# Optimization experiments

Hardware: AMD Instinct MI355X
Metric: run time of the kernel (lower is better)

Reference implementation:

```python
import jax, jax.numpy as jnp
import numpy as np

# hyperparameters (init_kwargs)
T = 0.1
MARGIN = 0.0
NEG_IOU = 0.5
K = 2              # pos_topk
WEIGHT = 1.0
EXPONENT = 2.0
NEG_SAMPLES = 512  # neg_samples_num
START_DNS_EPOCH = 1

# static problem sizes
B, SPB, TPS = 16, 2, 4          # videos, sentences/video, targets/sentence
N, C = 64, 256                  # clips, channels
S = B * SPB                     # total sentences = 32
M = S * TPS                     # total moments = 128


def setup_inputs() -> dict:
    key = jax.random.key(0)
    k1, k2, k3, k4 = jax.random.split(key, 4)
    return {
        "video_feats": jax.random.normal(k1, (S, C, N, N), jnp.float32),
        "sents_feats": jax.random.normal(k2, (S, C), jnp.float32),
        "num_sentences": jnp.full((B,), SPB, jnp.int32),
        "num_targets": jnp.full((S,), TPS, jnp.int32),
        "iou2d": jax.random.uniform(k3, (S, N, N), jnp.float32),
        "iou2ds": jax.random.uniform(k4, (M, N, N), jnp.float32),
        "mask2d": jnp.triu(jnp.ones((N, N), bool)),  # 2D-TAN valid-proposal mask
        "epoch": 2,
    }


def _normalize(x):
    return x / jnp.maximum(jnp.linalg.norm(x, axis=-1, keepdims=True), 1e-12)


def _loss_core(video_feats, sents_feats, iou2d, iou2ds,
               num_sentences, num_targets, mask2d, epoch):
    S_, C_, N_, _ = video_feats.shape
    B_ = num_sentences.shape[0]
    M_ = iou2ds.shape[0]
    P = N_ * (N_ + 1) // 2  # number of True in upper-triangular mask2d

    # masked_select(mask2d) -> gather flat proposal positions (static size P)
    flat_idx = jnp.nonzero(mask2d.reshape(-1), size=P)[0]
    vf = video_feats.reshape(S_, C_, N_ * N_)[:, :, flat_idx]        # (S,C,P)
    vf = _normalize(vf.transpose(0, 2, 1))                            # (S,P,C)
    _ = _normalize(sents_feats)                                       # normalized but unused downstream
    iou2d_f = iou2d.reshape(S_, -1)[:, flat_idx]                      # (S,P)
    iou2ds_f = iou2ds.reshape(M_, -1)[:, flat_idx]                    # (M,P)

    scatter_m2s = jnp.repeat(jnp.arange(S_), num_targets, total_repeat_length=M_)
    scatter_s2b = jnp.repeat(jnp.arange(B_), num_sentences, total_repeat_length=S_)
    scatter_b2s = jnp.concatenate([jnp.zeros((1,), jnp.int32),
                                   jnp.cumsum(num_sentences)[:-1].astype(jnp.int32)])

    # all (ref, pos) pairs within each sentence's num_targets*K topk slots (uniform -> static)
    nK = (M_ // S_) * K
    base = (jnp.arange(S_) * nK)[:, None, None]
    i = jnp.arange(nK)
    zero = jnp.zeros((nK,), jnp.int32)
    ref_idx = (base + i[None, :, None] + zero[None, None, :]).reshape(-1)   # (E,)
    pos_idx = (base + zero[None, :, None] + i[None, None, :]).reshape(-1)   # (E,)
    scatter_e2s = jnp.repeat(jnp.arange(S_), nK * nK)                        # (E,)

    # top-K proposals per moment by IoU
    topk_idx = jax.lax.top_k(iou2ds_f, K)[1]                                 # (M,K)
    allm = vf[scatter_m2s]                                                   # (M,P,C)
    topk_vf = jnp.take_along_axis(allm, topk_idx[:, :, None], axis=1)        # (M,K,C)
    pos_vf = topk_vf.reshape(M_ * K, C_)

    intra_pos = jnp.sum(pos_vf[ref_idx] * pos_vf[pos_idx], axis=-1)          # (E,)
    bank = vf[scatter_b2s].reshape(B_ * P, C_)                               # one sentence per video
    intra_all = pos_vf @ bank.T                                              # (M*K, B*P)

    # positive mask: own-video block, refined by iou2d > neg_iou
    own = scatter_s2b[:, None] == jnp.arange(B_)[None, :]                    # (S,B)
    s2v_pos = iou2d_f > NEG_IOU                                              # (S,P)
    pos_mask = jnp.where(own[:, :, None], s2v_pos[:, None, :], False).reshape(S_, B_ * P)

    if epoch >= START_DNS_EPOCH:
        # DNS: similarity-weighted negative sampling without replacement (Gumbel top-k)
        sim = (jnp.einsum('mkc,pc->mkp', topk_vf, bank).mean(axis=1) + 1.0) * 0.5   # (M,B*P)
        fused = jax.ops.segment_sum(sim, scatter_m2s, num_segments=S_)
        fused = fused / num_targets[:, None].astype(sim.dtype)                      # per-sentence mean
        fused = jnp.where(pos_mask, 0.0, fused ** EXPONENT)                          # (S,B*P)
        logw = jnp.where(fused > 0, jnp.log(jnp.maximum(fused, 1e-30)), -jnp.inf)
        u = jax.random.uniform(jax.random.key(42), fused.shape, minval=1e-7, maxval=1.0 - 1e-7)
        gumbel = -jnp.log(-jnp.log(u))
        samp_idx = jax.lax.top_k(logw + gumbel, NEG_SAMPLES)[1]                      # (S,NEG_SAMPLES)
        neg_mask = jnp.zeros((S_, B_ * P), jnp.float32).at[
            jnp.arange(S_)[:, None], samp_idx].set(1.0)
    else:
        neg_mask = (~pos_mask).astype(jnp.float32)

    # LogCrossEntropy (InfoNCE with explicit negative mask)
    all_e = intra_all[ref_idx]            # (E, B*P)
    neg_e = neg_mask[scatter_e2s]         # (E, B*P)
    pos_logit = (intra_pos - MARGIN) / T
    neg_sum = jnp.sum(jnp.exp(all_e / T) * neg_e, axis=-1)
    loss = jnp.mean(-(pos_logit - jnp.log(jnp.exp(pos_logit) + neg_sum)))
    return loss


def reference(video_feats, sents_feats, num_sentences, num_targets,
              iou2d, iou2ds, mask2d, epoch):
    loss = _loss_core(video_feats, sents_feats, iou2d, iou2ds,
                      num_sentences, num_targets, mask2d, epoch)
    return (loss * WEIGHT, loss)
```

## Files before the change

### kernel.cpp

```cpp
#include <hip/hip_runtime.h>
#include <math.h>
#include <stdint.h>

#define S_    32
#define BV_   16
#define M_    128
#define C_    256
#define NN    4096
#define P_    2080
#define BP    33280
#define NSAMP 512
#define EQCAP 2048

__device__ __forceinline__ uint32_t rotl32(uint32_t x, int n){ return (x<<n) | (x>>(32-n)); }

__device__ __forceinline__ void threefry2x32(uint32_t k0, uint32_t k1, uint32_t &x0, uint32_t &x1){
  uint32_t ks2 = k0 ^ k1 ^ 0x1BD11BDAu;
  x0 += k0; x1 += k1;
  #define TF_R(r) { x0 += x1; x1 = rotl32(x1, r); x1 ^= x0; }
  TF_R(13) TF_R(15) TF_R(26) TF_R(6)
  x0 += k1;  x1 += ks2 + 1u;
  TF_R(17) TF_R(29) TF_R(16) TF_R(24)
  x0 += ks2; x1 += k0 + 2u;
  TF_R(13) TF_R(15) TF_R(26) TF_R(6)
  x0 += k0;  x1 += k1 + 3u;
  TF_R(17) TF_R(29) TF_R(16) TF_R(24)
  x0 += k1;  x1 += ks2 + 4u;
  TF_R(13) TF_R(15) TF_R(26) TF_R(6)
  x0 += ks2; x1 += k0 + 5u;
  #undef TF_R
}

__device__ __forceinline__ void p_to_ij(int p, int &i, int &j){
  i = (int)((129.0f - sqrtf((float)(16641 - 8*p))) * 0.5f);
  while(64*(i+1) - ((i+1)*i)/2 <= p) ++i;
  while(64*i - (i*(i-1))/2 > p) --i;
  j = i + (p - (64*i - (i*(i-1))/2));
}

__global__ __launch_bounds__(256) void k_topk(const float* __restrict__ iou2ds,
                                              int* __restrict__ fpk){
  int m = blockIdx.x;
  const float* row = iou2ds + (size_t)m*NN;
  float v1=-1e30f, v2=-1e30f; int i1=0x7FFFFFFF, i2=0x7FFFFFFF;
  for(int f=threadIdx.x; f<NN; f+=256){
    int ti = f>>6, tj = f&63;
    if(tj < ti) continue;
    float v = row[f];
    if(v > v1 || (v == v1 && f < i1)){ v2=v1; i2=i1; v1=v; i1=f; }
    else if(v > v2 || (v == v2 && f < i2)){ v2=v; i2=f; }
  }
  __shared__ float sv1[256], sv2[256];
  __shared__ int   si1[256], si2[256];
  sv1[threadIdx.x]=v1; sv2[threadIdx.x]=v2; si1[threadIdx.x]=i1; si2[threadIdx.x]=i2;
  for(int stp=128; stp>0; stp>>=1){
    __syncthreads();
    if((int)threadIdx.x < stp){
      float a1=sv1[threadIdx.x], a2=sv2[threadIdx.x];
      int   x1=si1[threadIdx.x], x2=si2[threadIdx.x];
      float b1=sv1[threadIdx.x+stp], b2=sv2[threadIdx.x+stp];
      int   y1=si1[threadIdx.x+stp], y2=si2[threadIdx.x+stp];
      float m1v, m2v; int m1i, m2i;
      bool aTop = (a1 > b1) || (a1 == b1 && x1 < y1);
      if(aTop){
        m1v=a1; m1i=x1;
        if((a2 > b1) || (a2 == b1 && x2 < y1)){ m2v=a2; m2i=x2; } else { m2v=b1; m2i=y1; }
      } else {
        m1v=b1; m1i=y1;
        if((b2 > a1) || (b2 == a1 && y2 < x1)){ m2v=b2; m2i=y2; } else { m2v=a1; m2i=x1; }
      }
      sv1[threadIdx.x]=m1v; sv2[threadIdx.x]=m2v; si1[threadIdx.x]=m1i; si2[threadIdx.x]=m2i;
    }
  }
  __syncthreads();
  if(threadIdx.x==0){
    fpk[m*2+0] = si1[0];
    fpk[m*2+1] = si2[0];
  }
}

__global__ __launch_bounds__(256) void k_pos(const float* __restrict__ vfeat,
                                             const int* __restrict__ fpk,
                                             float* __restrict__ pos_vf,
                                             float* __restrict__ qsumT){
  int s = blockIdx.x;
  int c = threadIdx.x;
  __shared__ float wsum[4];
  __shared__ float s_inv;
  float qs = 0.f;
  for(int r=0; r<8; ++r){
    int row = s*8 + r;
    int fp = fpk[row];
    float v = vfeat[((size_t)s*C_ + c)*NN + fp];
    float ss = v*v;
    for(int o=32;o>0;o>>=1) ss += __shfl_down(ss, o, 64);
    if((c&63)==0) wsum[c>>6]=ss;
    __syncthreads();
    if(c==0){
      float tot = wsum[0]+wsum[1]+wsum[2]+wsum[3];
      s_inv = 1.0f / fmaxf(sqrtf(tot), 1e-12f);
    }
    __syncthreads();
    float pv = v * s_inv;
    pos_vf[(size_t)row*C_ + c] = pv;
    qs += pv;
  }
  qsumT[c*32 + s] = qs;
}

__global__ __launch_bounds__(256) void k_bank(const float* __restrict__ vfeat,
                                              float* __restrict__ bank){
  extern __shared__ char dyn_sm[];
  float* tile = (float*)dyn_sm;
  float* ssp  = (float*)dyn_sm + 256*65;
  float* invs = (float*)dyn_sm + 256*65 + 256;

  int i = blockIdx.x;
  int b = blockIdx.y;
  int t = threadIdx.x;
  int j = t & 63, cq = t >> 6;
  const float* basep = vfeat + (size_t)(2*b)*C_*NN + (size_t)i*64;

  float ssq = 0.f;
  for(int it=0; it<64; ++it){
    int cc = it*4 + cq;
    float v = basep[(size_t)cc*NN + j];
    tile[cc*65 + j] = v;
    ssq += v*v;
  }
  ssp[t] = ssq;
  __syncthreads();
  if(t < 64){
    float tot = ssp[t]+ssp[64+t]+ssp[128+t]+ssp[192+t];
    invs[t] = 1.0f/fmaxf(sqrtf(tot), 1e-12f);
  }
  __syncthreads();

  int start = 64*i - (i*(i-1))/2;
  for(int jj=i; jj<64; ++jj){
    size_t row = (size_t)b*P_ + start + (jj - i);
    bank[row*C_ + t] = tile[t*65 + jj] * invs[jj];
  }
}

__global__ __launch_bounds__(256) void k_fused_keys(const float* __restrict__ bank,
                                                    const float* __restrict__ qsumT,
                                                    const float* __restrict__ iou2d,
                                                    unsigned int* __restrict__ ukey){
  __shared__ float tile[32*257];
  const int t = threadIdx.x;
  const int j = blockIdx.x*256 + t;

  int bv = j / P_;
  int p  = j - bv*P_;
  int pi, pj; p_to_ij(p, pi, pj);
  int fp = pi*64 + pj;
  float iou0 = iou2d[(size_t)(2*bv)*NN + fp];
  float iou1 = iou2d[(size_t)(2*bv+1)*NN + fp];

  float acc[32];
  #pragma unroll
  for(int s=0;s<32;s++) acc[s]=0.f;

  for(int cb=0; cb<8; ++cb){
    __syncthreads();
    #pragma unroll
    for(int it=0; it<8; ++it){
      int idx = it*256 + t;
      int jj  = idx >> 3;
      int c4  = idx & 7;
      float4 v = ((const float4*)bank)[ (size_t)(blockIdx.x*256 + jj)*64 + cb*8 + c4 ];
      tile[(c4*4+0)*257 + jj]=v.x; tile[(c4*4+1)*257 + jj]=v.y;
      tile[(c4*4+2)*257 + jj]=v.z; tile[(c4*4+3)*257 + jj]=v.w;
    }
    __syncthreads();
    const float* qb = qsumT + cb*32*32;
    #pragma unroll 2
    for(int cc=0; cc<32; ++cc){
      float v = tile[cc*257 + t];
      const float* qc = qb + cc*32;
      #pragma unroll
      for(int s=0;s<32;s++) acc[s] = fmaf(qc[s], v, acc[s]);
    }
  }

  #pragma unroll 1
  for(int s=0;s<32;s++){
    float fz = 0.0625f*acc[s] + 0.5f;
    bool pos = ((s>>1)==bv) && (((s&1)?iou1:iou0) > 0.5f);
    float val = pos ? 0.f : fz*fz;
    float key;
    if(val > 0.f){
      float logw = logf(fmaxf(val, 1e-30f));
      unsigned int f = (unsigned int)(s*BP + j);
      const unsigned int HALF = 532480u;
      bool second = f >= HALF;
      uint32_t x0 = second ? (f - HALF) : f;
      uint32_t x1 = second ? f : (f + HALF);
      threefry2x32(0u, 42u, x0, x1);
      uint32_t bits = second ? x1 : x0;
      uint32_t fb = (bits >> 9) | 0x3f800000u;
      float f01 = __uint_as_float(fb) - 1.0f;
      const float mn = 1e-7f, mx = 1.0f - 1e-7f;
      float u = fmaxf(mn, f01*(mx-mn) + mn);
      float g = -logf(-logf(u));
      key = logw + g;
    } else {
      key = -INFINITY;
    }
    unsigned int kb = __float_as_uint(key);
    kb = (kb & 0x80000000u) ? ~kb : (kb | 0x80000000u);
    ukey[(size_t)s*BP + j] = kb;
  }
}

__global__ __launch_bounds__(1024) void k_select(const unsigned int* __restrict__ ukey,
                                                 int* __restrict__ neglist){
  extern __shared__ char dyn_sm[];
  unsigned int* row  = (unsigned int*)dyn_sm;
  unsigned int* hist = (unsigned int*)dyn_sm + BP;
  int* eqbuf = (int*)hist;
  __shared__ int s_wv[16];
  __shared__ unsigned int s_prefix;
  __shared__ int s_cntgt, s_need, s_eq;

  const int s = blockIdx.x;
  const int t = threadIdx.x;
  const int lane = t & 63;
  const int col  = t & 15;
  const unsigned int* grow = ukey + (size_t)s*BP;
  int* list = neglist + s*NSAMP;

  unsigned int prefix = 0, pmask = 0;
  int need = NSAMP, cnt_gt = 0;

  for(int lev=0; lev<4; ++lev){
    const int shift = 24 - 8*lev;
    for(int k=t; k<256*17; k+=1024) hist[k] = 0;
    __syncthreads();
    if(lev==0){
      for(int k=t; k<BP; k+=1024){
        unsigned int u = grow[k];
        row[k] = u;
        atomicAdd(&hist[(u >> 24)*17 + col], 1u);
      }
    } else {
      for(int k=t; k<BP; k+=1024){
        unsigned int u = row[k];
        if((u & pmask) == prefix)
          atomicAdd(&hist[((u >> shift) & 255u)*17 + col], 1u);
      }
    }
    __syncthreads();
    int v = 0; unsigned int h = 0;
    if(t < 256){
      const unsigned int* hr = hist + t*17;
      #pragma unroll
      for(int c=0;c<16;c++) h += hr[c];
      v = (int)h;
      #pragma unroll
      for(int off=1; off<64; off<<=1){
        int src = lane + off;
        int o = __shfl(v, (src<64)?src:lane, 64);
        v += (src<64)? o : 0;
      }
      if(lane==0) s_wv[t>>6] = v;
    }
    __syncthreads();
    if(t < 256){
      int wv4 = t>>6, tail = 0;
      for(int w2=wv4+1; w2<4; ++w2) tail += s_wv[w2];
      int Sb  = v + tail;
      int Sb1 = Sb - (int)h;
      if(Sb >= need && Sb1 < need){
        s_prefix = prefix | ((unsigned int)t << shift);
        s_cntgt  = cnt_gt + Sb1;
        s_need   = need - Sb1;
      }
    }
    __syncthreads();
    prefix = s_prefix; cnt_gt = s_cntgt; need = s_need;
    pmask |= (0xFFu << shift);
    __syncthreads();
  }

  const unsigned int ustar = prefix;
  const int quota = need;

  if(t==0) s_eq = 0;
  __syncthreads();

  int gtc = 0;
  for(int k=t; k<BP; k+=1024) gtc += (row[k] > ustar) ? 1 : 0;
  int vg = gtc;
  #pragma unroll
  for(int off=1; off<64; off<<=1){
    int src = lane - off;
    int o = __shfl(vg, (src>=0)?src:lane, 64);
    vg += (src>=0)? o : 0;
  }
  const int wv16 = t>>6;
  if(lane==63) s_wv[wv16] = vg;
  __syncthreads();
  int base2 = 0;
  for(int w2=0; w2<wv16; ++w2) base2 += s_wv[w2];
  int gi = base2 + vg - gtc;
  for(int k=t; k<BP; k+=1024){
    unsigned int u = row[k];
    if(u > ustar){
      list[gi++] = k;
    } else if(u == ustar){
      int e = atomicAdd(&s_eq, 1);
      if(e < EQCAP) eqbuf[e] = k;
    }
  }
  __syncthreads();
  const int eqn = s_eq;
  if(eqn <= EQCAP){
    for(int i=t; i<eqn; i+=1024){
      int ii = eqbuf[i];
      int r = 0;
      for(int j2=0; j2<eqn; ++j2) r += (eqbuf[j2] < ii) ? 1 : 0;
      if(r < quota) list[cnt_gt + r] = ii;
    }
  } else {
    if(t==0){
      int taken = 0;
      for(int idx=0; idx<BP && taken<quota; ++idx)
        if(row[idx]==ustar){ list[cnt_gt + taken] = idx; ++taken; }
    }
  }
}

__global__ __launch_bounds__(512) void k_negloss(const float* __restrict__ bank,
                                                 const float* __restrict__ pos_vf,
                                                 const int* __restrict__ neglist,
                                                 float* __restrict__ partial){
  int s = blockIdx.x;
  int t = threadIdx.x;
  __shared__ float pv[8][260];
  __shared__ float red[8][8];
  __shared__ float ns_s[8];
  for(int idx=t; idx<8*C_; idx+=512) pv[idx>>8][idx&255] = pos_vf[(size_t)(s*8)*C_ + idx];
  __syncthreads();
  int j = neglist[s*NSAMP + t];
  const float4* bp = (const float4*)(bank + (size_t)j*C_);
  float acc[8] = {0,0,0,0,0,0,0,0};
  for(int c4=0; c4<64; ++c4){
    float4 bv = bp[c4];
    #pragma unroll
    for(int a=0;a<8;a++){
      float4 pvv = *(const float4*)&pv[a][c4*4];
      acc[a] += bv.x*pvv.x + bv.y*pvv.y + bv.z*pvv.z + bv.w*pvv.w;
    }
  }
  float e[8];
  #pragma unroll
  for(int a=0;a<8;a++){
    float v = expf(acc[a]/0.1f);
    for(int o=32;o>0;o>>=1) v += __shfl_down(v, o, 64);
    e[a] = v;
  }
  int wv = t>>6;
  if((t&63)==0){
    #pragma unroll
    for(int a=0;a<8;a++) red[wv][a]=e[a];
  }
  __syncthreads();
  if(t < 8){
    float tot = 0.f;
    for(int w=0; w<8; w++) tot += red[w][t];
    ns_s[t] = tot;
  }
  __syncthreads();
  if(t < 64){
    int a = t>>3, b = t&7;
    float dot = 0.f;
    for(int c=0;c<C_;c++) dot += pv[a][c]*pv[b][c];
    float pl = dot/0.1f;
    float term = logf(expf(pl) + ns_s[a]) - pl;
    for(int o=32;o>0;o>>=1) term += __shfl_down(term, o, 64);
    if(t==0) partial[s]=term;
  }
}

__global__ void k_final(const float* __restrict__ partial, float* __restrict__ out){
  int t = threadIdx.x;
  float v = (t < 32) ? partial[t] : 0.f;
  for(int o=32;o>0;o>>=1) v += __shfl_down(v, o, 64);
  if(t==0){
    float loss = v / 2048.0f;
    out[0] = loss * 1.0f;
    out[1] = loss;
  }
}

extern "C" void kernel_launch(void* const* d_in, const int* in_sizes, int n_in,
                              void* d_out, int out_size, void* d_ws, size_t ws_size,
                              hipStream_t stream) {
  const float* video_feats = (const float*)d_in[0];
  const float* iou2d  = (const float*)d_in[4];
  const float* iou2ds = (const float*)d_in[5];

  const size_t o_fpk   = 0;
  const size_t o_pvf   = 1024;
  const size_t o_qsT   = 263168;
  const size_t o_bank  = 295936;
  const size_t o_ukey  = 34374656;
  const size_t o_list  = 38634496;
  const size_t o_part  = 38700032;
  const size_t NEED    = 38700160;
  if (ws_size < NEED) return;

  char* w = (char*)d_ws;
  int*          fpk     = (int*)(w + o_fpk);
  float*        pos_vf  = (float*)(w + o_pvf);
  float*        qsumT   = (float*)(w + o_qsT);
  float*        bank    = (float*)(w + o_bank);
  unsigned int* ukey    = (unsigned int*)(w + o_ukey);
  int*          neglist = (int*)(w + o_list);
  float*        part    = (float*)(w + o_part);
  float*        out     = (float*)d_out;

  const int SEL_LDS = (BP + 256*17) * 4;
  static bool attr_set = false;
  if(!attr_set){
    (void)hipFuncSetAttribute((const void*)k_select,
                              hipFuncAttributeMaxDynamicSharedMemorySize,
                              SEL_LDS);
    (void)hipFuncSetAttribute((const void*)k_bank,
                              hipFuncAttributeMaxDynamicSharedMemorySize,
                              (256*65 + 256 + 64) * 4);
    attr_set = true;
  }

  k_topk<<<128, 256, 0, stream>>>(iou2ds, fpk);
  k_pos<<<32, 256, 0, stream>>>(video_feats, fpk, pos_vf, qsumT);
  k_bank<<<dim3(64,16), 256, (256*65 + 256 + 64) * 4, stream>>>(video_feats, bank);
  k_fused_keys<<<130, 256, 0, stream>>>(bank, qsumT, iou2d, ukey);
  k_select<<<32, 1024, SEL_LDS, stream>>>(ukey, neglist);
  k_negloss<<<32, 512, 0, stream>>>(bank, pos_vf, neglist, part);
  k_final<<<1, 64, 0, stream>>>(part, out);
}
```

Baseline: 155.3 us.

## Fuse seven kernels into three: prep, bank+keys, select+negloss with atomic final

Merges topk with positive-feature normalisation, computes the Gumbel sampling keys directly from the LDS tile inside the bank kernel, and folds negative-loss computation and the final reduction into the selection kernel using an atomic counter. This removes four launches, the re-read of the normalised bank for key generation, and the global neglist round-trip. The trade-off is that the key phase in k_bankkeys now does far more redundant per-block work (1024 blocks, many with idle lanes in the triangle), and the final reduction relies on a last-block atomic pattern.

Measured after the change: 165.2 us. 1.06x slower.

```diff
diff --git a/kernel.cpp b/kernel.cpp
--- a/kernel.cpp
+++ b/kernel.cpp
@@ -31,94 +31,90 @@
   #undef TF_R
 }
 
-__device__ __forceinline__ void p_to_ij(int p, int &i, int &j){
-  i = (int)((129.0f - sqrtf((float)(16641 - 8*p))) * 0.5f);
-  while(64*(i+1) - ((i+1)*i)/2 <= p) ++i;
-  while(64*i - (i*(i-1))/2 > p) --i;
-  j = i + (p - (64*i - (i*(i-1))/2));
-}
-
-__global__ __launch_bounds__(256) void k_topk(const float* __restrict__ iou2ds,
-                                              int* __restrict__ fpk){
-  int m = blockIdx.x;
-  const float* row = iou2ds + (size_t)m*NN;
-  float v1=-1e30f, v2=-1e30f; int i1=0x7FFFFFFF, i2=0x7FFFFFFF;
-  for(int f=threadIdx.x; f<NN; f+=256){
-    int ti = f>>6, tj = f&63;
-    if(tj < ti) continue;
-    float v = row[f];
-    if(v > v1 || (v == v1 && f < i1)){ v2=v1; i2=i1; v1=v; i1=f; }
-    else if(v > v2 || (v == v2 && f < i2)){ v2=v; i2=f; }
-  }
+__global__ __launch_bounds__(256) void k_prep(const float* __restrict__ iou2ds,
+                                              const float* __restrict__ vfeat,
+                                              float* __restrict__ pos_vf,
+                                              float* __restrict__ qsumT,
+                                              int* __restrict__ counter){
+  const int s = blockIdx.x;
+  const int t = threadIdx.x;
   __shared__ float sv1[256], sv2[256];
   __shared__ int   si1[256], si2[256];
-  sv1[threadIdx.x]=v1; sv2[threadIdx.x]=v2; si1[threadIdx.x]=i1; si2[threadIdx.x]=i2;
-  for(int stp=128; stp>0; stp>>=1){
-    __syncthreads();
-    if((int)threadIdx.x < stp){
-      float a1=sv1[threadIdx.x], a2=sv2[threadIdx.x];
-      int   x1=si1[threadIdx.x], x2=si2[threadIdx.x];
-      float b1=sv1[threadIdx.x+stp], b2=sv2[threadIdx.x+stp];
-      int   y1=si1[threadIdx.x+stp], y2=si2[threadIdx.x+stp];
-      float m1v, m2v; int m1i, m2i;
-      bool aTop = (a1 > b1) || (a1 == b1 && x1 < y1);
-      if(aTop){
-        m1v=a1; m1i=x1;
-        if((a2 > b1) || (a2 == b1 && x2 < y1)){ m2v=a2; m2i=x2; } else { m2v=b1; m2i=y1; }
-      } else {
-        m1v=b1; m1i=y1;
-        if((b2 > a1) || (b2 == a1 && y2 < x1)){ m2v=b2; m2i=y2; } else { m2v=a1; m2i=x1; }
-      }
-      sv1[threadIdx.x]=m1v; sv2[threadIdx.x]=m2v; si1[threadIdx.x]=m1i; si2[threadIdx.x]=m2i;
-    }
-  }
-  __syncthreads();
-  if(threadIdx.x==0){
-    fpk[m*2+0] = si1[0];
-    fpk[m*2+1] = si2[0];
-  }
-}
-
-__global__ __launch_bounds__(256) void k_pos(const float* __restrict__ vfeat,
-                                             const int* __restrict__ fpk,
-                                             float* __restrict__ pos_vf,
-                                             float* __restrict__ qsumT){
-  int s = blockIdx.x;
-  int c = threadIdx.x;
+  __shared__ int   fpk_s[8];
   __shared__ float wsum[4];
   __shared__ float s_inv;
+
+  if(s==0 && t==0) *counter = 0;
+
+  for(int q=0; q<4; ++q){
+    const float* row = iou2ds + (size_t)(s*4 + q)*NN;
+    float v1=-1e30f, v2=-1e30f; int i1=0x7FFFFFFF, i2=0x7FFFFFFF;
+    for(int f=t; f<NN; f+=256){
+      int ti = f>>6, tj = f&63;
+      if(tj < ti) continue;
+      float v = row[f];
+      if(v > v1 || (v == v1 && f < i1)){ v2=v1; i2=i1; v1=v; i1=f; }
+      else if(v > v2 || (v == v2 && f < i2)){ v2=v; i2=f; }
+    }
+    sv1[t]=v1; sv2[t]=v2; si1[t]=i1; si2[t]=i2;
+    for(int stp=128; stp>0; stp>>=1){
+      __syncthreads();
+      if(t < stp){
+        float a1=sv1[t], a2=sv2[t]; int x1=si1[t], x2=si2[t];
+        float b1=sv1[t+stp], b2=sv2[t+stp]; int y1=si1[t+stp], y2=si2[t+stp];
+        float m1v, m2v; int m1i, m2i;
+        bool aTop = (a1 > b1) || (a1 == b1 && x1 < y1);
+        if(aTop){
+          m1v=a1; m1i=x1;
+          if((a2 > b1) || (a2 == b1 && x2 < y1)){ m2v=a2; m2i=x2; } else { m2v=b1; m2i=y1; }
+        } else {
+          m1v=b1; m1i=y1;
+          if((b2 > a1) || (b2 == a1 && y2 < x1)){ m2v=b2; m2i=y2; } else { m2v=a1; m2i=x1; }
+        }
+        sv1[t]=m1v; sv2[t]=m2v; si1[t]=m1i; si2[t]=m2i;
+      }
+    }
+    __syncthreads();
+    if(t==0){ fpk_s[q*2+0]=si1[0]; fpk_s[q*2+1]=si2[0]; }
+    __syncthreads();
+  }
+
+  float v[8];
+  #pragma unroll
+  for(int r=0;r<8;r++) v[r] = vfeat[((size_t)s*C_ + t)*NN + fpk_s[r]];
+
   float qs = 0.f;
   for(int r=0; r<8; ++r){
-    int row = s*8 + r;
-    int fp = fpk[row];
-    float v = vfeat[((size_t)s*C_ + c)*NN + fp];
-    float ss = v*v;
+    float ss = v[r]*v[r];
     for(int o=32;o>0;o>>=1) ss += __shfl_down(ss, o, 64);
-    if((c&63)==0) wsum[c>>6]=ss;
-    __syncthreads();
-    if(c==0){
+    if((t&63)==0) wsum[t>>6]=ss;
+    __syncthreads();
+    if(t==0){
       float tot = wsum[0]+wsum[1]+wsum[2]+wsum[3];
       s_inv = 1.0f / fmaxf(sqrtf(tot), 1e-12f);
     }
     __syncthreads();
-    float pv = v * s_inv;
-    pos_vf[(size_t)row*C_ + c] = pv;
+    float pv = v[r] * s_inv;
+    pos_vf[(size_t)(s*8+r)*C_ + t] = pv;
     qs += pv;
   }
-  qsumT[c*32 + s] = qs;
+  qsumT[t*32 + s] = qs;
 }
 
-__global__ __launch_bounds__(256) void k_bank(const float* __restrict__ vfeat,
-                                              float* __restrict__ bank){
+__global__ __launch_bounds__(256) void k_bankkeys(const float* __restrict__ vfeat,
+                                                  const float* __restrict__ qsumT,
+                                                  const float* __restrict__ iou2d,
+                                                  float* __restrict__ bank,
+                                                  unsigned int* __restrict__ ukey){
   extern __shared__ char dyn_sm[];
   float* tile = (float*)dyn_sm;
   float* ssp  = (float*)dyn_sm + 256*65;
   float* invs = (float*)dyn_sm + 256*65 + 256;
 
-  int i = blockIdx.x;
-  int b = blockIdx.y;
-  int t = threadIdx.x;
-  int j = t & 63, cq = t >> 6;
+  const int i = blockIdx.x;
+  const int b = blockIdx.y;
+  const int t = threadIdx.x;
+  const int j = t & 63, cq = t >> 6;
   const float* basep = vfeat + (size_t)(2*b)*C_*NN + (size_t)i*64;
 
   float ssq = 0.f;
@@ -136,100 +132,87 @@
   }
   __syncthreads();
 
-  int start = 64*i - (i*(i-1))/2;
+  const int start = 64*i - (i*(i-1))/2;
   for(int jj=i; jj<64; ++jj){
     size_t row = (size_t)b*P_ + start + (jj - i);
     bank[row*C_ + t] = tile[t*65 + jj] * invs[jj];
   }
+
+  const int lane = t & 63;
+  const int sbase = __builtin_amdgcn_readfirstlane((t >> 6) * 8);
+  float acc[8];
+  #pragma unroll
+  for(int k=0;k<8;k++) acc[k]=0.f;
+  #pragma unroll 4
+  for(int cc=0; cc<256; ++cc){
+    float v = tile[cc*65 + lane];
+    const float* qc = qsumT + cc*32 + sbase;
+    #pragma unroll
+    for(int k=0;k<8;k++) acc[k] = fmaf(qc[k], v, acc[k]);
+  }
+
+  if(lane >= i){
+    const int jg = b*P_ + start + (lane - i);
+    const int fp = i*64 + lane;
+    const float iou0 = iou2d[(size_t)(2*b)*NN + fp];
+    const float iou1 = iou2d[(size_t)(2*b+1)*NN + fp];
+    const float inv_j = invs[lane];
+    #pragma unroll 1
+    for(int k=0;k<8;k++){
+      const int sIdx = sbase + k;
+      float fz = 0.0625f*(acc[k]*inv_j) + 0.5f;
+      bool pos = ((sIdx>>1)==b) && (((sIdx&1)?iou1:iou0) > 0.5f);
+      float val = pos ? 0.f : fz*fz;
+      float key;
+      if(val > 0.f){
+        float logw = logf(fmaxf(val, 1e-30f));
+        unsigned int f = (unsigned int)(sIdx*BP + jg);
+        const unsigned int HALF = 532480u;
+        bool second = f >= HALF;
+        uint32_t x0 = second ? (f - HALF) : f;
+        uint32_t x1 = second ? f : (f + HALF);
+        threefry2x32(0u, 42u, x0, x1);
+        uint32_t bits = second ? x1 : x0;
+        uint32_t fb = (bits >> 9) | 0x3f800000u;
+        float f01 = __uint_as_float(fb) - 1.0f;
+        const float mn = 1e-7f, mx = 1.0f - 1e-7f;
+        float u = fmaxf(mn, f01*(mx-mn) + mn);
+        float g = -logf(-logf(u));
+        key = logw + g;
+      } else {
+        key = -INFINITY;
+      }
+      unsigned int kb = __float_as_uint(key);
+      kb = (kb & 0x80000000u) ? ~kb : (kb | 0x80000000u);
+      ukey[(size_t)sIdx*BP + jg] = kb;
+    }
+  }
 }
 
-__global__ __launch_bounds__(256) void k_fused_keys(const float* __restrict__ bank,
-                                                    const float* __restrict__ qsumT,
-                                                    const float* __restrict__ iou2d,
-                                                    unsigned int* __restrict__ ukey){
-  __shared__ float tile[32*257];
-  const int t = threadIdx.x;
-  const int j = blockIdx.x*256 + t;
-
-  int bv = j / P_;
-  int p  = j - bv*P_;
-  int pi, pj; p_to_ij(p, pi, pj);
-  int fp = pi*64 + pj;
-  float iou0 = iou2d[(size_t)(2*bv)*NN + fp];
-  float iou1 = iou2d[(size_t)(2*bv+1)*NN + fp];
-
-  float acc[32];
-  #pragma unroll
-  for(int s=0;s<32;s++) acc[s]=0.f;
-
-  for(int cb=0; cb<8; ++cb){
-    __syncthreads();
-    #pragma unroll
-    for(int it=0; it<8; ++it){
-      int idx = it*256 + t;
-      int jj  = idx >> 3;
-      int c4  = idx & 7;
-      float4 v = ((const float4*)bank)[ (size_t)(blockIdx.x*256 + jj)*64 + cb*8 + c4 ];
-      tile[(c4*4+0)*257 + jj]=v.x; tile[(c4*4+1)*257 + jj]=v.y;
-      tile[(c4*4+2)*257 + jj]=v.z; tile[(c4*4+3)*257 + jj]=v.w;
-    }
-    __syncthreads();
-    const float* qb = qsumT + cb*32*32;
-    #pragma unroll 2
-    for(int cc=0; cc<32; ++cc){
-      float v = tile[cc*257 + t];
-      const float* qc = qb + cc*32;
-      #pragma unroll
-      for(int s=0;s<32;s++) acc[s] = fmaf(qc[s], v, acc[s]);
-    }
-  }
-
-  #pragma unroll 1
-  for(int s=0;s<32;s++){
-    float fz = 0.0625f*acc[s] + 0.5f;
-    bool pos = ((s>>1)==bv) && (((s&1)?iou1:iou0) > 0.5f);
-    float val = pos ? 0.f : fz*fz;
-    float key;
-    if(val > 0.f){
-      float logw = logf(fmaxf(val, 1e-30f));
-      unsigned int f = (unsigned int)(s*BP + j);
-      const unsigned int HALF = 532480u;
-      bool second = f >= HALF;
-      uint32_t x0 = second ? (f - HALF) : f;
-      uint32_t x1 = second ? f : (f + HALF);
-      threefry2x32(0u, 42u, x0, x1);
-      uint32_t bits = second ? x1 : x0;
-      uint32_t fb = (bits >> 9) | 0x3f800000u;
-      float f01 = __uint_as_float(fb) - 1.0f;
-      const float mn = 1e-7f, mx = 1.0f - 1e-7f;
-      float u = fmaxf(mn, f01*(mx-mn) + mn);
-      float g = -logf(-logf(u));
-      key = logw + g;
-    } else {
-      key = -INFINITY;
-    }
-    unsigned int kb = __float_as_uint(key);
-    kb = (kb & 0x80000000u) ? ~kb : (kb | 0x80000000u);
-    ukey[(size_t)s*BP + j] = kb;
-  }
-}
-
-__global__ __launch_bounds__(1024) void k_select(const unsigned int* __restrict__ ukey,
-                                                 int* __restrict__ neglist){
+__global__ __launch_bounds__(1024) void k_selneg(const unsigned int* __restrict__ ukey,
+                                                 const float* __restrict__ bank,
+                                                 const float* __restrict__ pos_vf,
+                                                 float* __restrict__ partial,
+                                                 int* __restrict__ counter,
+                                                 float* __restrict__ out){
   extern __shared__ char dyn_sm[];
   unsigned int* row  = (unsigned int*)dyn_sm;
   unsigned int* hist = (unsigned int*)dyn_sm + BP;
-  int* eqbuf = (int*)hist;
+  int* list_lds = (int*)hist;
+  int* eqbuf    = (int*)hist + 512;
+  float* pv     = (float*)dyn_sm;
+  float* hibuf  = (float*)dyn_sm + 4096;
   __shared__ int s_wv[16];
   __shared__ unsigned int s_prefix;
   __shared__ int s_cntgt, s_need, s_eq;
+  __shared__ float red[8][8];
+  __shared__ float ns_s[8];
 
   const int s = blockIdx.x;
   const int t = threadIdx.x;
   const int lane = t & 63;
   const int col  = t & 15;
   const unsigned int* grow = ukey + (size_t)s*BP;
-  int* list = neglist + s*NSAMP;
 
   unsigned int prefix = 0, pmask = 0;
   int need = NSAMP, cnt_gt = 0;
@@ -308,7 +291,7 @@
   for(int k=t; k<BP; k+=1024){
     unsigned int u = row[k];
     if(u > ustar){
-      list[gi++] = k;
+      list_lds[gi++] = k;
     } else if(u == ustar){
       int e = atomicAdd(&s_eq, 1);
       if(e < EQCAP) eqbuf[e] = k;
@@ -317,54 +300,58 @@
   __syncthreads();
   const int eqn = s_eq;
   if(eqn <= EQCAP){
-    for(int i=t; i<eqn; i+=1024){
-      int ii = eqbuf[i];
+    for(int i2=t; i2<eqn; i2+=1024){
+      int ii = eqbuf[i2];
       int r = 0;
       for(int j2=0; j2<eqn; ++j2) r += (eqbuf[j2] < ii) ? 1 : 0;
-      if(r < quota) list[cnt_gt + r] = ii;
+      if(r < quota) list_lds[cnt_gt + r] = ii;
     }
   } else {
     if(t==0){
       int taken = 0;
       for(int idx=0; idx<BP && taken<quota; ++idx)
-        if(row[idx]==ustar){ list[cnt_gt + taken] = idx; ++taken; }
-    }
-  }
-}
-
-__global__ __launch_bounds__(512) void k_negloss(const float* __restrict__ bank,
-                                                 const float* __restrict__ pos_vf,
-                                                 const int* __restrict__ neglist,
-                                                 float* __restrict__ partial){
-  int s = blockIdx.x;
-  int t = threadIdx.x;
-  __shared__ float pv[8][260];
-  __shared__ float red[8][8];
-  __shared__ float ns_s[8];
-  for(int idx=t; idx<8*C_; idx+=512) pv[idx>>8][idx&255] = pos_vf[(size_t)(s*8)*C_ + idx];
-  __syncthreads();
-  int j = neglist[s*NSAMP + t];
-  const float4* bp = (const float4*)(bank + (size_t)j*C_);
+        if(row[idx]==ustar){ list_lds[cnt_gt + taken] = idx; ++taken; }
+    }
+  }
+  __syncthreads();
+
+  for(int idx=t; idx<8*C_; idx+=1024){
+    int a = idx>>8, c = idx&255;
+    pv[a*260 + c] = pos_vf[(size_t)(s*8)*C_ + idx];
+  }
+  __syncthreads();
+
+  const int t0 = t & 511, half = t >> 9;
+  const int jn = list_lds[t0];
+  const float4* bp = (const float4*)(bank + (size_t)jn*C_ + half*128);
   float acc[8] = {0,0,0,0,0,0,0,0};
-  for(int c4=0; c4<64; ++c4){
+  for(int c4=0; c4<32; ++c4){
     float4 bv = bp[c4];
     #pragma unroll
     for(int a=0;a<8;a++){
-      float4 pvv = *(const float4*)&pv[a][c4*4];
-      acc[a] += bv.x*pvv.x + bv.y*pvv.y + bv.z*pvv.z + bv.w*pvv.w;
-    }
-  }
-  float e[8];
-  #pragma unroll
-  for(int a=0;a<8;a++){
-    float v = expf(acc[a]/0.1f);
-    for(int o=32;o>0;o>>=1) v += __shfl_down(v, o, 64);
-    e[a] = v;
-  }
-  int wv = t>>6;
-  if((t&63)==0){
+      const float* pva = pv + a*260 + half*128 + c4*4;
+      acc[a] += bv.x*pva[0] + bv.y*pva[1] + bv.z*pva[2] + bv.w*pva[3];
+    }
+  }
+  if(half==1){
     #pragma unroll
-    for(int a=0;a<8;a++) red[wv][a]=e[a];
+    for(int a=0;a<8;a++) hibuf[t0*8 + a] = acc[a];
+  }
+  __syncthreads();
+  if(t < 512){
+    float e[8];
+    #pragma unroll
+    for(int a=0;a<8;a++){
+      float accf = acc[a] + hibuf[t0*8 + a];
+      float v = expf(accf/0.1f);
+      for(int o=32;o>0;o>>=1) v += __shfl_down(v, o, 64);
+      e[a] = v;
+    }
+    int wv = t>>6;
+    if((t&63)==0){
+      #pragma unroll
+      for(int a=0;a<8;a++) red[wv][a]=e[a];
+    }
   }
   __syncthreads();
   if(t < 8){
@@ -373,25 +360,27 @@
     ns_s[t] = tot;
   }
   __syncthreads();
+
   if(t < 64){
-    int a = t>>3, b = t&7;
+    int a = t>>3, b2 = t&7;
     float dot = 0.f;
-    for(int c=0;c<C_;c++) dot += pv[a][c]*pv[b][c];
+    for(int c=0;c<C_;c++) dot += pv[a*260+c]*pv[b2*260+c];
     float pl = dot/0.1f;
     float term = logf(expf(pl) + ns_s[a]) - pl;
     for(int o=32;o>0;o>>=1) term += __shfl_down(term, o, 64);
-    if(t==0) partial[s]=term;
-  }
-}
-
-__global__ void k_final(const float* __restrict__ partial, float* __restrict__ out){
-  int t = threadIdx.x;
-  float v = (t < 32) ? partial[t] : 0.f;
-  for(int o=32;o>0;o>>=1) v += __shfl_down(v, o, 64);
-  if(t==0){
-    float loss = v / 2048.0f;
-    out[0] = loss * 1.0f;
-    out[1] = loss;
+    if(t==0){
+      atomicExch(&partial[s], term);
+      __threadfence();
+      int old = atomicAdd(counter, 1);
+      if(old == 31){
+        __threadfence();
+        float sum = 0.f;
+        for(int i2=0;i2<32;i2++) sum += atomicAdd(&partial[i2], 0.0f);
+        float loss = sum / 2048.0f;
+        out[0] = loss * 1.0f;
+        out[1] = loss;
+      }
+    }
   }
 }
 
@@ -402,43 +391,36 @@
   const float* iou2d  = (const float*)d_in[4];
   const float* iou2ds = (const float*)d_in[5];
 
-  const size_t o_fpk   = 0;
-  const size_t o_pvf   = 1024;
-  const size_t o_qsT   = 263168;
-  const size_t o_bank  = 295936;
-  const size_t o_ukey  = 34374656;
-  const size_t o_list  = 38634496;
-  const size_t o_part  = 38700032;
-  const size_t NEED    = 38700160;
+  const size_t o_pvf   = 0;
+  const size_t o_qsT   = 262144;
+  const size_t o_bank  = 294912;
+  const size_t o_ukey  = 34373632;
+  const size_t o_part  = 38633472;
+  const size_t o_cnt   = 38633600;
+  const size_t NEED    = 38633728;
   if (ws_size < NEED) return;
 
   char* w = (char*)d_ws;
-  int*          fpk     = (int*)(w + o_fpk);
   float*        pos_vf  = (float*)(w + o_pvf);
   float*        qsumT   = (float*)(w + o_qsT);
   float*        bank    = (float*)(w + o_bank);
   unsigned int* ukey    = (unsigned int*)(w + o_ukey);
-  int*          neglist = (int*)(w + o_list);
   float*        part    = (float*)(w + o_part);
+  int*          counter = (int*)(w + o_cnt);
   float*        out     = (float*)d_out;
 
+  const int BK_LDS  = (256*65 + 256 + 64) * 4;
   const int SEL_LDS = (BP + 256*17) * 4;
   static bool attr_set = false;
   if(!attr_set){
-    (void)hipFuncSetAttribute((const void*)k_select,
-                              hipFuncAttributeMaxDynamicSharedMemorySize,
-                              SEL_LDS);
-    (void)hipFuncSetAttribute((const void*)k_bank,
-                              hipFuncAttributeMaxDynamicSharedMemorySize,
-                              (256*65 + 256 + 64) * 4);
+    (void)hipFuncSetAttribute((const void*)k_bankkeys,
+                              hipFuncAttributeMaxDynamicSharedMemorySize, BK_LDS);
+    (void)hipFuncSetAttribute((const void*)k_selneg,
+                              hipFuncAttributeMaxDynamicSharedMemorySize, SEL_LDS);
     attr_set = true;
   }
 
-  k_topk<<<128, 256, 0, stream>>>(iou2ds, fpk);
-  k_pos<<<32, 256, 0, stream>>>(video_feats, fpk, pos_vf, qsumT);
-  k_bank<<<dim3(64,16), 256, (256*65 + 256 + 64) * 4, stream>>>(video_feats, bank);
-  k_fused_keys<<<130, 256, 0, stream>>>(bank, qsumT, iou2d, ukey);
-  k_select<<<32, 1024, SEL_LDS, stream>>>(ukey, neglist);
-  k_negloss<<<32, 512, 0, stream>>>(bank, pos_vf, neglist, part);
-  k_final<<<1, 64, 0, stream>>>(part, out);
+  k_prep<<<32, 256, 0, stream>>>(iou2ds, video_feats, pos_vf, qsumT, counter);
+  k_bankkeys<<<dim3(64,16), 256, BK_LDS, stream>>>(video_feats, qsumT, iou2d, bank, ukey);
+  k_selneg<<<32, 1024, SEL_LDS, stream>>>(ukey, bank, pos_vf, part, counter, out);
 }
```
